# Kernel optimization log

Hardware: AMD Instinct MI355X
Metric: run time of the kernel (lower is better)

Reference implementation:

```python
import jax, jax.numpy as jnp
import numpy as np

M = 256      # num memories in bnn_history
D = 7686     # input_size (2 agent one-hot + 7680 embedding + 4 scalars)
H = 256      # NEAT hidden nodes
O = 4        # NEAT output nodes
N = D + H + O  # total nodes in dense weight matrix


def setup_inputs() -> dict:
    key = jax.random.key(0)
    ks = jax.random.split(key, 8)
    inv_sqrt_d = 1.0 / np.sqrt(D).astype(np.float32)
    return {
        "input_matrix": jax.random.normal(ks[0], (M, D), jnp.float32),
        "Wq": jax.random.normal(ks[1], (D, D), jnp.float32) * inv_sqrt_d,
        "bq": jnp.zeros((D,), jnp.float32),
        "Wk": jax.random.normal(ks[2], (D, D), jnp.float32) * inv_sqrt_d,
        "bk": jnp.zeros((D,), jnp.float32),
        "Wv": jax.random.normal(ks[3], (D, D), jnp.float32) * inv_sqrt_d,
        "bv": jnp.zeros((D,), jnp.float32),
        "weight_mu": jax.random.normal(ks[4], (N, N), jnp.float32) * 0.01,
        "weight_sigma": jnp.full((N, N), 0.1, jnp.float32),  # build_network inits sigma to 0.1
        "bias_mu": jnp.zeros((H + O,), jnp.float32),
        "bias_sigma": jnp.full((H + O,), 0.1, jnp.float32),
        "eps_w": jax.random.normal(ks[5], (N, N), jnp.float32),
        "eps_b": jax.random.normal(ks[6], (H + O,), jnp.float32),
    }


def reference(input_matrix, Wq, bq, Wk, bk, Wv, bv,
              weight_mu, weight_sigma, bias_mu, bias_sigma, eps_w, eps_b):
    # --- attention over memory rows (nn.Linear applies x @ W.T + b) ---
    Q = input_matrix @ Wq.T + bq            # [M, D]
    K = input_matrix @ Wk.T + bk            # [M, D]
    V = input_matrix @ Wv.T + bv            # [M, D]
    scale = 1.0 / jnp.sqrt(jnp.asarray(D, input_matrix.dtype))
    attn = jax.nn.softmax((Q @ K.T) * scale, axis=-1)  # [M, M]
    context = (attn @ V).mean(axis=0)       # [D] pooled attended context

    # --- Bayesian reparameterized genome weights / biases ---
    W = weight_mu + weight_sigma * eps_w    # [N, N], W[i, j] = weight of edge i->j
    b = bias_mu + bias_sigma * eps_b        # [H+O]

    # --- topological NEAT-style evaluation: inputs, then hidden, then outputs ---
    values0 = jnp.zeros((N,), input_matrix.dtype).at[:D].set(context)

    def step(values, j):
        col = jax.lax.dynamic_slice_in_dim(W, j, 1, axis=1)[:, 0]  # incoming weights of node j
        pre = values @ col + b[j - D]        # sum aggregation + bias
        return values.at[j].set(jnp.tanh(pre)), None

    values, _ = jax.lax.scan(step, values0, jnp.arange(D, N))
    return values[-O:]                       # output node activations
```

## Files before the change

### kernel.cpp

```cpp
#include <hip/hip_runtime.h>
#include <hip/hip_bf16.h>
#include <type_traits>

#define DIN   7686
#define NNODE 7946
#define HOUT  260
#define KP    8192
#define BROW  1036

typedef __attribute__((ext_vector_type(8))) short bf16x8;
typedef __attribute__((ext_vector_type(4))) float f32x4;
typedef __attribute__((ext_vector_type(2))) float f32x2;

__device__ __forceinline__ unsigned int f2b(float f) {
  union { float f; unsigned int u; } v; v.f = f;
  return (v.u + 0x7FFFu + ((v.u >> 16) & 1u)) >> 16;
}
__device__ __forceinline__ unsigned int pack2(float lo, float hi) {
  unsigned int r;
  asm("v_cvt_pk_bf16_f32 %0, %1, %2" : "=v"(r) : "v"(lo), "v"(hi));
  return r;
}
__device__ __forceinline__ float b2f(unsigned short h) {
  union { unsigned int u; float f; } v; v.u = ((unsigned int)h) << 16; return v.f;
}
__device__ __forceinline__ float readlane_f(float v, int lane) {
  return __uint_as_float(__builtin_amdgcn_readlane(__float_as_uint(v), lane));
}

__global__ void prep_x2(const float* __restrict__ X, char* __restrict__ XbT2)
{
  const int m = blockIdx.x, t = threadIdx.x;
  const float* row = X + (size_t)m * DIN;
  const int i16 = m >> 4;
#pragma unroll
  for (int c2 = 0; c2 < 4; ++c2) {
    const int k8 = (c2 * 256 + t) * 8;
    float f[8];
    if (k8 + 8 <= DIN) {
#pragma unroll
      for (int h = 0; h < 4; ++h) {
        float2 v = *(const float2*)(row + k8 + h * 2);
        f[h * 2] = v.x; f[h * 2 + 1] = v.y;
      }
    } else {
#pragma unroll
      for (int h = 0; h < 8; ++h) f[h] = (k8 + h < DIN) ? row[k8 + h] : 0.f;
    }
    uint4 o;
    o.x = pack2(f[0], f[1]); o.y = pack2(f[2], f[3]);
    o.z = pack2(f[4], f[5]); o.w = pack2(f[6], f[7]);
    const int kc = k8 >> 7, kk = k8 & 127, ks = kk >> 5, hq = (kk & 31) >> 3;
    const int lane = (m & 15) + (hq << 4);
    char* dst = XbT2 + ((((size_t)kc * 16 + i16) * 4 + ks) << 10) + lane * 16;
    *(uint4*)dst = o;
  }
}

__global__ __launch_bounds__(512, 4)
void gemm_qk8(const char* __restrict__ XbT2,
              const float* __restrict__ Wq, const float* __restrict__ Wk,
              unsigned short* __restrict__ PQK)
{
  const int nt = blockIdx.x, mat = blockIdx.y, zg = blockIdx.z;
  const float* W = mat ? Wk : Wq;
  const int n0 = nt * 32;
  const int tid = threadIdx.x, l = tid & 63, wv = tid >> 6;
  const int lm = l & 15, hq = l >> 4;

  __shared__ __align__(16) unsigned short Bp[32 * BROW];

  const long long DD = (long long)DIN * DIN;

  f32x4 acc[2][2] = {};
  bf16x8 A0[2], A1[2], A2[2];
  f32x4 F[16];

  long long rb[4];
#pragma unroll
  for (int r = 0; r < 4; ++r) {
    int grow = n0 + wv * 4 + r; if (grow > DIN - 1) grow = DIN - 1;
    rb[r] = (long long)grow * DIN;
  }

#define LOADW(z_) {                                                       \
    const int k0_ = (z_) * 1024;                                          \
    _Pragma("unroll")                                                     \
    for (int r_ = 0; r_ < 4; ++r_)                                        \
      _Pragma("unroll")                                                   \
      for (int c_ = 0; c_ < 4; ++c_) {                                    \
        long long gi_ = rb[r_] + k0_ + c_ * 256 + l * 4;                  \
        if (gi_ > DD - 4) gi_ = DD - 4;       \
        F[r_ * 4 + c_] = __builtin_nontemporal_load((const f32x4*)(W + gi_)); \
      } }

#define WRITEW() {                                                        \
    _Pragma("unroll")                                                     \
    for (int r_ = 0; r_ < 4; ++r_) {                                      \
      unsigned short* dr_ = &Bp[(wv * 4 + r_) * BROW];                    \
      _Pragma("unroll")                                                   \
      for (int c_ = 0; c_ < 4; ++c_) {                                    \
        f32x4 v_ = F[r_ * 4 + c_];                                        \
        uint2 o_; o_.x = pack2(v_[0], v_[1]); o_.y = pack2(v_[2], v_[3]); \
        *(uint2*)(dr_ + c_ * 256 + l * 4) = o_;                           \
      } } }

#define LA(dst, z_, s_) {                                                 \
    const int kc_ = (z_) * 8 + ((s_) >> 2), ks_ = (s_) & 3;               \
    const char* b_ = XbT2 +                                               \
        ((((size_t)kc_ * 16 + 2 * wv) * 4 + ks_) << 10) + l * 16;         \
    dst[0] = *(const bf16x8*)b_;                                          \
    dst[1] = *(const bf16x8*)(b_ + 4096); }

#define STEP(Ar, s_) {                                                    \
    bf16x8 b0_ = *(const bf16x8*)&Bp[lm * BROW + (s_) * 32 + hq * 8];     \
    bf16x8 b1_ = *(const bf16x8*)&Bp[(16 + lm) * BROW + (s_) * 32 + hq * 8]; \
    acc[0][0] = __builtin_amdgcn_mfma_f32_16x16x32_bf16(Ar[0], b0_, acc[0][0], 0, 0, 0); \
    acc[0][1] = __builtin_amdgcn_mfma_f32_16x16x32_bf16(Ar[0], b1_, acc[0][1], 0, 0, 0); \
    acc[1][0] = __builtin_amdgcn_mfma_f32_16x16x32_bf16(Ar[1], b0_, acc[1][0], 0, 0, 0); \
    acc[1][1] = __builtin_amdgcn_mfma_f32_16x16x32_bf16(Ar[1], b1_, acc[1][1], 0, 0, 0); }

#pragma unroll 1
  for (int h = 0; h < 2; ++h) {
    const int z = zg + h * 4;

    if (h) __syncthreads();

    LOADW(z)
    WRITEW()
    __syncthreads();

    LA(A0, z, 0) LA(A1, z, 1) LA(A2, z, 2)
#pragma unroll 1
    for (int su = 0; su < 30; su += 3) {
      STEP(A0, su + 0)
      if (su + 3 < 32) LA(A0, z, su + 3)
      STEP(A1, su + 1)
      if (su + 4 < 32) LA(A1, z, su + 4)
      STEP(A2, su + 2)
      if (su + 5 < 32) LA(A2, z, su + 5)
    }
    STEP(A0, 30)
    STEP(A1, 31)
  }
#undef LOADW
#undef WRITEW
#undef LA
#undef STEP

  unsigned short* Cp = PQK + (size_t)(mat * 4 + zg) * 256 * KP;
#pragma unroll
  for (int i = 0; i < 2; ++i) {
    const int r0 = (2 * wv + i) * 16 + hq * 4;
#pragma unroll
    for (int j = 0; j < 2; ++j) {
      const int col = n0 + j * 16 + lm;
#pragma unroll
      for (int q = 0; q < 4; ++q)
        Cp[(size_t)(r0 + q) * KP + col] = (unsigned short)f2b(acc[i][j][q]);
    }
  }
}

__global__ void reduce_qk4(const unsigned short* __restrict__ PQK,
                           const float* __restrict__ bq, const float* __restrict__ bk,
                           unsigned short* __restrict__ Qbf, unsigned short* __restrict__ Kbf)
{
  const int mat = blockIdx.y;
  const int c = blockIdx.x * 128 + threadIdx.x;
  const float* bias = mat ? bk : bq;
  const bool valid = c < DIN;
  const float bb = valid ? bias[c] : 0.f;
  const unsigned short* P0 = PQK + ((size_t)(mat * 4 + 0) * 256) * KP + c;
  const unsigned short* P1 = PQK + ((size_t)(mat * 4 + 1) * 256) * KP + c;
  const unsigned short* P2 = PQK + ((size_t)(mat * 4 + 2) * 256) * KP + c;
  const unsigned short* P3 = PQK + ((size_t)(mat * 4 + 3) * 256) * KP + c;
  unsigned short* O = (mat ? Kbf : Qbf) + c;
#pragma unroll 4
  for (int r = 0; r < 256; ++r) {
    float v = b2f(P0[(size_t)r * KP]) + b2f(P1[(size_t)r * KP]) +
              b2f(P2[(size_t)r * KP]) + b2f(P3[(size_t)r * KP]) + bb;
    if (!valid) v = 0.f;
    O[(size_t)r * KP] = (unsigned short)f2b(v);
  }
}

__global__ __launch_bounds__(512)
void gemm_logits(const unsigned short* __restrict__ Qbf,
                 const unsigned short* __restrict__ Kbf, float* __restrict__ LP)
{
  const int qr = blockIdx.x & 1, qc = blockIdx.x >> 1, z = blockIdx.z;
  const int tid = threadIdx.x, lane = tid & 63, wv = tid >> 6;
  const int lm = lane & 15, lq = (lane >> 4) * 8;
  const int rowBase = qr * 128 + (wv & 3) * 32;
  const int colBase = qc * 128 + (wv >> 2) * 64;
  const int k0 = z * 512;
  f32x4 acc[2][4] = {};
#pragma unroll 4
  for (int ks = 0; ks < 16; ++ks) {
    bf16x8 a[2], b[4];
#pragma unroll
    for (int i = 0; i < 2; ++i)
      a[i] = *(const bf16x8*)(Qbf + (size_t)(rowBase + i * 16 + lm) * KP + k0 + ks * 32 + lq);
#pragma unroll
    for (int j = 0; j < 4; ++j)
      b[j] = *(const bf16x8*)(Kbf + (size_t)(colBase + j * 16 + lm) * KP + k0 + ks * 32 + lq);
#pragma unroll
    for (int i = 0; i < 2; ++i)
#pragma unroll
      for (int j = 0; j < 4; ++j)
        acc[i][j] = __builtin_amdgcn_mfma_f32_16x16x32_bf16(a[i], b[j], acc[i][j], 0, 0, 0);
  }
  float* out = LP + (size_t)z * 65536;
#pragma unroll
  for (int i = 0; i < 2; ++i) {
    const int r0 = rowBase + i * 16 + (lane >> 4) * 4;
#pragma unroll
    for (int j = 0; j < 4; ++j) {
      const int col = colBase + j * 16 + lm;
#pragma unroll
      for (int q = 0; q < 4; ++q)
        out[(size_t)(r0 + q) * 256 + col] = acc[i][j][q];
    }
  }
}

__global__ void softmax_fused(const float* __restrict__ LP, float* __restrict__ abar)
{
  __shared__ float red[8];
  const int m = blockIdx.x, t = threadIdx.x;
  float v = 0.f;
#pragma unroll
  for (int zz = 0; zz < 16; ++zz) v += LP[(size_t)zz * 65536 + m * 256 + t];
  const float scale = 1.0f / sqrtf((float)DIN);
  float mx = v;
#pragma unroll
  for (int o = 32; o >= 1; o >>= 1) mx = fmaxf(mx, __shfl_xor(mx, o, 64));
  if ((t & 63) == 0) red[t >> 6] = mx;
  __syncthreads();
  mx = fmaxf(fmaxf(red[0], red[1]), fmaxf(red[2], red[3]));
  float e = __expf((v - mx) * scale);
  float s = e;
#pragma unroll
  for (int o = 32; o >= 1; o >>= 1) s += __shfl_xor(s, o, 64);
  if ((t & 63) == 0) red[4 + (t >> 6)] = s;
  __syncthreads();
  s = red[4] + red[5] + red[6] + red[7];
  atomicAdd(&abar[t], e * (1.0f / 256.0f) / s);
}

__global__ void y_kernel(const float* __restrict__ X, const float* __restrict__ abar,
                         float* __restrict__ y)
{
  __shared__ float ab[256];
  ab[threadIdx.x] = abar[threadIdx.x];
  __syncthreads();
  const int c = blockIdx.x * 256 + threadIdx.x;
  if (c >= DIN) return;
  float s = 0.f;
#pragma unroll 8
  for (int m = 0; m < 256; ++m) s += ab[m] * X[(size_t)m * DIN + c];
  y[c] = s;
}

__global__ __launch_bounds__(512)
void ctx_mv(const float* __restrict__ Wv, const float* __restrict__ y,
            const float* __restrict__ bv, float* __restrict__ ctx)
{
  const int wv = threadIdx.x >> 6, l = threadIdx.x & 63;
  const int row = blockIdx.x * 8 + wv;
  if (row >= DIN) return;
  const float* wr_ = Wv + (size_t)row * DIN;
  float s = 0.f;
#pragma unroll 5
  for (int it = 0; it < 30; ++it) {
    const int k = it * 256 + l * 4;
    f32x4 w4 = __builtin_nontemporal_load((const f32x4*)(wr_ + k));
    float4 y4 = *(const float4*)(y + k);
    s = fmaf(w4[0], y4.x, s);
    s = fmaf(w4[1], y4.y, s);
    s = fmaf(w4[2], y4.z, s);
    s = fmaf(w4[3], y4.w, s);
  }
  if (l < 6) s += wr_[7680 + l] * y[7680 + l];
#pragma unroll
  for (int o = 32; o >= 1; o >>= 1) s += __shfl_xor(s, o, 64);
  if (l == 0) ctx[row] = s + bv[row];
}

__global__ void base_kernel(const float* __restrict__ mu, const float* __restrict__ sg,
                            const float* __restrict__ ep, const float* __restrict__ ctx,
                            float* __restrict__ base)
{
  const int j = threadIdx.x;
  if (j >= HOUT) return;
  const int i0 = blockIdx.x * 31;
  const int i1 = min(i0 + 31, DIN);
  float acc = 0.f;
#pragma unroll 4
  for (int i = i0; i < i1; ++i) {
    const size_t idx = (size_t)i * NNODE + DIN + j;
    acc = fmaf(ctx[i], fmaf(sg[idx], ep[idx], mu[idx]), acc);
  }
  atomicAdd(&base[j], acc);
}

__global__ void ws_kernel(const float* __restrict__ mu, const float* __restrict__ sg,
                          const float* __restrict__ ep, float* __restrict__ WsG)
{
  const int t = blockIdx.x;
  const int j = threadIdx.x;
  if (j >= HOUT) return;
  const size_t idx = (size_t)(DIN + t) * NNODE + DIN + j;
  WsG[t * HOUT + j] = fmaf(sg[idx], ep[idx], mu[idx]);
}

__global__ __launch_bounds__(64, 1)
void scan2(const float* __restrict__ WsG, const float* __restrict__ base,
           const float* __restrict__ bmu, const float* __restrict__ bsg,
           const float* __restrict__ epb, float* __restrict__ out)
{
  __shared__ __align__(16) float tile[32 * HOUT + 128];
  const int l = threadIdx.x;

  float a0, a1, a2, a3, a4;
  {
    int j = l;       a0 = base[j] + bmu[j] + bsg[j] * epb[j];
    j = l + 64;      a1 = base[j] + bmu[j] + bsg[j] * epb[j];
    j = l + 128;     a2 = base[j] + bmu[j] + bsg[j] * epb[j];
    j = l + 192;     a3 = base[j] + bmu[j] + bsg[j] * epb[j];
    j = l + 256;     a4 = (j < HOUT) ? (base[j] + bmu[j] + bsg[j] * epb[j]) : 0.f;
  }

  float4 stg[33];
  auto LOADT = [&](int tb) {
    const int nfl = ((tb == 8) ? 4 : 32) * HOUT;
    const float* src = WsG + tb * 32 * HOUT;
#pragma unroll
    for (int c = 0; c < 33; ++c) {
      const int o = c * 256 + l * 4;
      if (o < nfl) stg[c] = *(const float4*)(src + o);
    }
  };
  auto WRITET = [&](int tb) {
    const int nfl = ((tb == 8) ? 4 : 32) * HOUT;
#pragma unroll
    for (int c = 0; c < 33; ++c) {
      const int o = c * 256 + l * 4;
      if (o < nfl) *(float4*)&tile[o] = stg[c];
    }
  };

  float w0, w1, w2, w3, w4;
  auto PRER = [&](int trow) {
    const float* tr = tile + trow * HOUT;
    w0 = tr[l]; w1 = tr[l + 64]; w2 = tr[l + 128]; w3 = tr[l + 192]; w4 = tr[l + 256];
  };

  auto inner = [&](auto Bc, int tb, int nrows) {
    constexpr int B = Bc.value;
    for (int tt = 0; tt < nrows; ++tt) {
      const int t = tb * 32 + tt;
      float pre;
      if constexpr (B == 0) pre = readlane_f(a0, t & 63);
      else if constexpr (B == 1) pre = readlane_f(a1, t & 63);
      else if constexpr (B == 2) pre = readlane_f(a2, t & 63);
      else if constexpr (B == 3) pre = readlane_f(a3, t & 63);
      else pre = readlane_f(a4, t & 63);
      const float pc = fminf(fmaxf(pre, -12.f), 12.f);
      const float e = __expf(2.f * pc);
      const float vt = 1.f - 2.f / (e + 1.f);
      if (t >= 256 && l == 0) out[t - 256] = vt;
      if (l > t)            a0 = fmaf(vt, w0, a0);
      if (l + 64 > t)       a1 = fmaf(vt, w1, a1);
      if (l + 128 > t)      a2 = fmaf(vt, w2, a2);
      if (l + 192 > t)      a3 = fmaf(vt, w3, a3);
      if (l + 256 > t && l + 256 < HOUT) a4 = fmaf(vt, w4, a4);
      if (tt + 1 < nrows) PRER(tt + 1);
    }
  };

  LOADT(0); WRITET(0); PRER(0);

#define TILE_STEP(tb, B, nr)                                    \
  { if ((tb) < 8) LOADT((tb) + 1);                              \
    inner(std::integral_constant<int, B>{}, (tb), (nr));        \
    if ((tb) < 8) { WRITET((tb) + 1); PRER(0); } }

  TILE_STEP(0, 0, 32)
  TILE_STEP(1, 0, 32)
  TILE_STEP(2, 1, 32)
  TILE_STEP(3, 1, 32)
  TILE_STEP(4, 2, 32)
  TILE_STEP(5, 2, 32)
  TILE_STEP(6, 3, 32)
  TILE_STEP(7, 3, 32)
  TILE_STEP(8, 4, 4)
#undef TILE_STEP
}

extern "C" void kernel_launch(void* const* d_in, const int* in_sizes, int n_in,
                              void* d_out, int out_size, void* d_ws, size_t ws_size,
                              hipStream_t stream)
{
  const float* X   = (const float*)d_in[0];
  const float* Wq  = (const float*)d_in[1];
  const float* bq  = (const float*)d_in[2];
  const float* Wk  = (const float*)d_in[3];
  const float* bk  = (const float*)d_in[4];
  const float* Wv  = (const float*)d_in[5];
  const float* bv  = (const float*)d_in[6];
  const float* wmu = (const float*)d_in[7];
  const float* wsg = (const float*)d_in[8];
  const float* bmu = (const float*)d_in[9];
  const float* bsg = (const float*)d_in[10];
  const float* epw = (const float*)d_in[11];
  const float* epb = (const float*)d_in[12];

  char* p = (char*)d_ws;
  auto alloc = [&](size_t bytes) -> char* {
    char* r = p;
    p += (bytes + 255) & ~(size_t)255;
    return r;
  };
  char* XbT2 = alloc((size_t)64 * 65536);
  unsigned short* PQK = (unsigned short*)alloc((size_t)8 * 256 * KP * 2);
  unsigned short* Qbf = (unsigned short*)alloc((size_t)256 * KP * 2);
  unsigned short* Kbf = (unsigned short*)alloc((size_t)256 * KP * 2);
  float* LP   = (float*)alloc((size_t)16 * 65536 * 4);
  float* abar = (float*)alloc(256 * 4);
  float* y    = (float*)alloc(7686 * 4);
  float* ctx  = (float*)alloc(7686 * 4);
  float* base = (float*)alloc(HOUT * 4);
  float* WsG  = (float*)alloc((size_t)HOUT * HOUT * 4 + 1024);

  prep_x2<<<dim3(256), dim3(256), 0, stream>>>(X, XbT2);
  (void)hipMemsetAsync(abar, 0, 256 * 4, stream);
  (void)hipMemsetAsync(base, 0, HOUT * 4, stream);

  gemm_qk8<<<dim3(241, 2, 4), dim3(512), 0, stream>>>(XbT2, Wq, Wk, PQK);
  reduce_qk4<<<dim3(64, 2), dim3(128), 0, stream>>>(PQK, bq, bk, Qbf, Kbf);
  gemm_logits<<<dim3(4, 1, 16), dim3(512), 0, stream>>>(Qbf, Kbf, LP);
  softmax_fused<<<dim3(256), dim3(256), 0, stream>>>(LP, abar);
  y_kernel<<<dim3(31), dim3(256), 0, stream>>>(X, abar, y);
  ctx_mv<<<dim3(961), dim3(512), 0, stream>>>(Wv, y, bv, ctx);
  base_kernel<<<dim3(256), dim3(320), 0, stream>>>(wmu, wsg, epw, ctx, base);
  ws_kernel<<<dim3(260), dim3(320), 0, stream>>>(wmu, wsg, epw, WsG);
  scan2<<<dim3(1), dim3(64), 0, stream>>>(WsG, base, bmu, bsg, epb, (float*)d_out);
}
```

Measured before the change: 378.7 us.

## Drop split-K in Q/K projection GEMM and fuse bias into epilogue

The Q/K projection GEMM stops splitting K four ways across blocks. Each block now loops over all eight K chunks and writes bias-added bf16 results straight into Qbf/Kbf, so the partial-sum buffer and the reduce kernel go away. This removes the partial-buffer writes and reads and one kernel launch, but the grid shrinks from 1928 to 482 blocks, each doing four times the serial work. That may leave the GPU's compute units underused. Two memsets are added to zero the padding in Qbf/Kbf.

Result: faster. 350.1 us (-7.5%).

```diff
diff --git a/kernel.cpp b/kernel.cpp
--- a/kernel.cpp
+++ b/kernel.cpp
@@ -58,12 +58,15 @@
 }
 
 __global__ __launch_bounds__(512, 4)
-void gemm_qk8(const char* __restrict__ XbT2,
+void gemm_qk9(const char* __restrict__ XbT2,
               const float* __restrict__ Wq, const float* __restrict__ Wk,
-              unsigned short* __restrict__ PQK)
-{
-  const int nt = blockIdx.x, mat = blockIdx.y, zg = blockIdx.z;
+              const float* __restrict__ bq, const float* __restrict__ bk,
+              unsigned short* __restrict__ Qbf, unsigned short* __restrict__ Kbf)
+{
+  const int nt = blockIdx.x, mat = blockIdx.y;
   const float* W = mat ? Wk : Wq;
+  const float* bias = mat ? bk : bq;
+  unsigned short* Out = mat ? Kbf : Qbf;
   const int n0 = nt * 32;
   const int tid = threadIdx.x, l = tid & 63, wv = tid >> 6;
   const int lm = l & 15, hq = l >> 4;
@@ -121,10 +124,8 @@
     acc[1][1] = __builtin_amdgcn_mfma_f32_16x16x32_bf16(Ar[1], b1_, acc[1][1], 0, 0, 0); }
 
 #pragma unroll 1
-  for (int h = 0; h < 2; ++h) {
-    const int z = zg + h * 4;
-
-    if (h) __syncthreads();
+  for (int z = 0; z < 8; ++z) {
+    if (z) __syncthreads();
 
     LOADW(z)
     WRITEW()
@@ -148,40 +149,19 @@
 #undef LA
 #undef STEP
 
-  unsigned short* Cp = PQK + (size_t)(mat * 4 + zg) * 256 * KP;
 #pragma unroll
   for (int i = 0; i < 2; ++i) {
     const int r0 = (2 * wv + i) * 16 + hq * 4;
 #pragma unroll
     for (int j = 0; j < 2; ++j) {
       const int col = n0 + j * 16 + lm;
-#pragma unroll
-      for (int q = 0; q < 4; ++q)
-        Cp[(size_t)(r0 + q) * KP + col] = (unsigned short)f2b(acc[i][j][q]);
-    }
-  }
-}
-
-__global__ void reduce_qk4(const unsigned short* __restrict__ PQK,
-                           const float* __restrict__ bq, const float* __restrict__ bk,
-                           unsigned short* __restrict__ Qbf, unsigned short* __restrict__ Kbf)
-{
-  const int mat = blockIdx.y;
-  const int c = blockIdx.x * 128 + threadIdx.x;
-  const float* bias = mat ? bk : bq;
-  const bool valid = c < DIN;
-  const float bb = valid ? bias[c] : 0.f;
-  const unsigned short* P0 = PQK + ((size_t)(mat * 4 + 0) * 256) * KP + c;
-  const unsigned short* P1 = PQK + ((size_t)(mat * 4 + 1) * 256) * KP + c;
-  const unsigned short* P2 = PQK + ((size_t)(mat * 4 + 2) * 256) * KP + c;
-  const unsigned short* P3 = PQK + ((size_t)(mat * 4 + 3) * 256) * KP + c;
-  unsigned short* O = (mat ? Kbf : Qbf) + c;
-#pragma unroll 4
-  for (int r = 0; r < 256; ++r) {
-    float v = b2f(P0[(size_t)r * KP]) + b2f(P1[(size_t)r * KP]) +
-              b2f(P2[(size_t)r * KP]) + b2f(P3[(size_t)r * KP]) + bb;
-    if (!valid) v = 0.f;
-    O[(size_t)r * KP] = (unsigned short)f2b(v);
+      const float bb = (col < DIN) ? bias[col] : 0.f;
+#pragma unroll
+      for (int q = 0; q < 4; ++q) {
+        const float v = acc[i][j][q] + bb;
+        Out[(size_t)(r0 + q) * KP + col] = (col < DIN) ? (unsigned short)f2b(v) : 0;
+      }
+    }
   }
 }
 
@@ -424,7 +404,6 @@
     return r;
   };
   char* XbT2 = alloc((size_t)64 * 65536);
-  unsigned short* PQK = (unsigned short*)alloc((size_t)8 * 256 * KP * 2);
   unsigned short* Qbf = (unsigned short*)alloc((size_t)256 * KP * 2);
   unsigned short* Kbf = (unsigned short*)alloc((size_t)256 * KP * 2);
   float* LP   = (float*)alloc((size_t)16 * 65536 * 4);
@@ -437,9 +416,10 @@
   prep_x2<<<dim3(256), dim3(256), 0, stream>>>(X, XbT2);
   (void)hipMemsetAsync(abar, 0, 256 * 4, stream);
   (void)hipMemsetAsync(base, 0, HOUT * 4, stream);
-
-  gemm_qk8<<<dim3(241, 2, 4), dim3(512), 0, stream>>>(XbT2, Wq, Wk, PQK);
-  reduce_qk4<<<dim3(64, 2), dim3(128), 0, stream>>>(PQK, bq, bk, Qbf, Kbf);
+  (void)hipMemsetAsync(Qbf, 0, (size_t)256 * KP * 2, stream);
+  (void)hipMemsetAsync(Kbf, 0, (size_t)256 * KP * 2, stream);
+
+  gemm_qk9<<<dim3(241, 2), dim3(512), 0, stream>>>(XbT2, Wq, Wk, bq, bk, Qbf, Kbf);
   gemm_logits<<<dim3(4, 1, 16), dim3(512), 0, stream>>>(Qbf, Kbf, LP);
   softmax_fused<<<dim3(256), dim3(256), 0, stream>>>(LP, abar);
   y_kernel<<<dim3(31), dim3(256), 0, stream>>>(X, abar, y);
```
